# Kernel optimization log

Hardware: AMD Instinct MI355X
Metric: run time of the kernel (lower is better)

The kernel has to match this reference:

```python
import jax, jax.numpy as jnp
import numpy as np

B, P, DE, DD, DA = 256, 196, 2048, 512, 512

def setup_inputs() -> dict:
    key = jax.random.key(0)
    ks = jax.random.split(key, 8)
    s_enc = 1.0 / np.sqrt(DE)
    s_dec = 1.0 / np.sqrt(DD)
    s_att = 1.0 / np.sqrt(DA)
    return {
        "encoder_out": jax.random.normal(ks[0], (B, P, DE), dtype=jnp.float32),
        "decoder_hidden": jax.random.normal(ks[1], (B, DD), dtype=jnp.float32),
        "W_enc": jax.random.uniform(ks[2], (DE, DA), jnp.float32, -s_enc, s_enc),
        "b_enc": jax.random.uniform(ks[3], (DA,), jnp.float32, -s_enc, s_enc),
        "W_dec": jax.random.uniform(ks[4], (DD, DA), jnp.float32, -s_dec, s_dec),
        "b_dec": jax.random.uniform(ks[5], (DA,), jnp.float32, -s_dec, s_dec),
        "W_full": jax.random.uniform(ks[6], (DA, 1), jnp.float32, -s_att, s_att),
        "b_full": jax.random.uniform(ks[7], (1,), jnp.float32, -s_att, s_att),
    }

def reference(encoder_out, decoder_hidden, W_enc, b_enc, W_dec, b_dec, W_full, b_full):
    # att1: [B,P,DA]; att2: [B,DA]
    att1 = jnp.einsum('bpe,ea->bpa', encoder_out, W_enc) + b_enc
    att2 = decoder_hidden @ W_dec + b_dec
    # broadcast add + relu + project to scalar score per position
    att = jnp.einsum('bpa,a->bp', jax.nn.relu(att1 + att2[:, None, :]), W_full[:, 0]) + b_full[0]
    alpha = jax.nn.softmax(att, axis=1)  # [B,P]
    context_vector = jnp.einsum('bpe,bp->be', encoder_out, alpha)  # [B,DE]
    return (context_vector, alpha)
```

## Files before the change

### kernel.cpp

```cpp
#include <hip/hip_runtime.h>
#include <hip/hip_bf16.h>
#include <cstddef>

#define B_   256
#define P_   196
#define DE_  2048
#define DD_  512
#define DA_  512
#define M_   (B_*P_)

#define BM   64
#define KT   32
#define NKT  (DE_/KT)

typedef __attribute__((ext_vector_type(4))) float f32x4;
typedef __attribute__((ext_vector_type(8))) short s16x8;

static __device__ __forceinline__ short f2bf(float x) {
    __hip_bfloat16 h = __float2bfloat16(x);
    return *reinterpret_cast<short*>(&h);
}

__global__ __launch_bounds__(256) void pack_wenc(
        const float* __restrict__ W, __hip_bfloat16* __restrict__ out) {
    __shared__ float lds[KT][DA_];
    const int kt = blockIdx.x;
    const int t  = threadIdx.x;
#pragma unroll
    for (int i = 0; i < 64; ++i) {
        int e = i * 256 + t;
        int k = e >> 9, n = e & 511;
        lds[k][n] = W[(size_t)(kt * KT + k) * DA_ + n];
    }
    __syncthreads();
    short* o = reinterpret_cast<short*>(out) + (size_t)kt * (32 * 64 * 8);
#pragma unroll
    for (int i = 0; i < 8; ++i) {
        int idx  = i * 256 + t;
        int gf   = idx >> 6;
        int lane = idx & 63;
        int g = lane >> 4, c = lane & 15;
        s16x8 w;
#pragma unroll
        for (int j = 0; j < 8; ++j)
            w[j] = f2bf(lds[g * 8 + j][gf * 16 + c]);
        *reinterpret_cast<s16x8*>(o + (size_t)idx * 8) = w;
    }
}

__global__ __launch_bounds__(512) void att2_kernel(
        const float* __restrict__ dh, const float* __restrict__ W_dec,
        const float* __restrict__ b_dec, const float* __restrict__ b_enc,
        float* __restrict__ att2p) {
    __shared__ float s_dh[DD_];
    const int b = blockIdx.x;
    const int a = threadIdx.x;
    s_dh[a] = dh[(size_t)b * DD_ + a];
    __syncthreads();
    float acc = 0.f;
#pragma unroll 8
    for (int k = 0; k < DD_; ++k)
        acc += s_dh[k] * W_dec[(size_t)k * DA_ + a];
    att2p[(size_t)b * DA_ + a] = acc + b_dec[a] + b_enc[a];
}

__global__ __launch_bounds__(256, 2) void gemm_att(
        const float* __restrict__ enc, const __hip_bfloat16* __restrict__ Bp,
        const float* __restrict__ att2p, const float* __restrict__ Wfull,
        const float* __restrict__ bfull, float* __restrict__ att) {
    __shared__ __hip_bfloat16 a_lds0[BM * KT];
    __shared__ __hip_bfloat16 a_lds1[BM * KT];
    __shared__ float red[BM][4];

    const int tid  = threadIdx.x;
    const int wave = tid >> 6;
    const int lane = tid & 63;
    const int g    = lane >> 4;
    const int c    = lane & 15;
    const int block_row = blockIdx.x * BM;
    const int nbase = wave * 128;
    const int slot8 = (g ^ ((c >> 1) & 3)) * 8;

    const int ar = tid >> 2;
    const int aq = tid & 3;
    const int a_woff = ar * KT + (aq ^ ((ar >> 1) & 3)) * 8;
    const float* ap = enc + (size_t)(block_row + ar) * DE_ + aq * 8;

    const s16x8* bp = reinterpret_cast<const s16x8*>(Bp) + (size_t)(wave * 8) * 64 + lane;

    f32x4 acc[4][8] = {};
    f32x4 pX0, pX1, pY0, pY1;
    s16x8 bf[8];

#define ISSUE_A(v0, v1, T) do {                                         \
        const int tt_ = (T) > 63 ? 63 : (T);                            \
        v0 = *reinterpret_cast<const f32x4*>(ap + tt_ * KT);            \
        v1 = *reinterpret_cast<const f32x4*>(ap + tt_ * KT + 4);        \
    } while (0)

#define ISSUE_BF(T) do {                                                \
        _Pragma("unroll")                                               \
        for (int nt_ = 0; nt_ < 8; ++nt_)                               \
            bf[nt_] = bp[((size_t)(T) * 32 + nt_) * 64];                \
    } while (0)

#define STORE_A(dst, v0, v1) do {                                       \
        s16x8 w_;                                                       \
        w_[0]=f2bf((v0).x); w_[1]=f2bf((v0).y); w_[2]=f2bf((v0).z); w_[3]=f2bf((v0).w); \
        w_[4]=f2bf((v1).x); w_[5]=f2bf((v1).y); w_[6]=f2bf((v1).z); w_[7]=f2bf((v1).w); \
        *reinterpret_cast<s16x8*>((dst) + a_woff) = w_;                 \
    } while (0)

#define AFRAGS_MFMA(abuf) do {                                          \
        s16x8 af[4];                                                    \
        _Pragma("unroll")                                               \
        for (int mt_ = 0; mt_ < 4; ++mt_)                               \
            af[mt_] = *reinterpret_cast<const s16x8*>((abuf) + (mt_*16 + c) * KT + slot8); \
        _Pragma("unroll")                                               \
        for (int nt_ = 0; nt_ < 8; ++nt_)                               \
            _Pragma("unroll")                                           \
            for (int mt_ = 0; mt_ < 4; ++mt_)                           \
                acc[mt_][nt_] = __builtin_amdgcn_mfma_f32_16x16x32_bf16(\
                                    af[mt_], bf[nt_], acc[mt_][nt_], 0, 0, 0); \
    } while (0)

#define BAR() do {                                                      \
        asm volatile("s_waitcnt lgkmcnt(0)" ::: "memory");              \
        __builtin_amdgcn_s_barrier();                                   \
        __builtin_amdgcn_sched_barrier(0);                              \
    } while (0)

    ISSUE_A(pX0, pX1, 0);
    ISSUE_A(pY0, pY1, 1);
    ISSUE_BF(0);
    STORE_A(a_lds0, pX0, pX1);
    ISSUE_A(pX0, pX1, 2);
    BAR();

#pragma clang loop unroll(disable)
    for (int t = 0; t < 62; t += 2) {
        STORE_A(a_lds1, pY0, pY1);
        ISSUE_A(pY0, pY1, t + 3);
        AFRAGS_MFMA(a_lds0);
        ISSUE_BF(t + 1);
        BAR();
        STORE_A(a_lds0, pX0, pX1);
        ISSUE_A(pX0, pX1, t + 4);
        AFRAGS_MFMA(a_lds1);
        ISSUE_BF(t + 2);
        BAR();
    }
    STORE_A(a_lds1, pY0, pY1);
    AFRAGS_MFMA(a_lds0);
    ISSUE_BF(63);
    BAR();
    AFRAGS_MFMA(a_lds1);

    const int b0    = block_row / P_;
    const int b1    = min(b0 + 1, B_ - 1);
    const int split = (b0 + 1) * P_;
    float wf[8], a20[8], a21[8];
#pragma unroll
    for (int nt = 0; nt < 8; ++nt) {
        const int n = nbase + nt * 16 + c;
        wf[nt]  = Wfull[n];
        a20[nt] = att2p[(size_t)b0 * DA_ + n];
        a21[nt] = att2p[(size_t)b1 * DA_ + n];
    }
#pragma unroll
    for (int mt = 0; mt < 4; ++mt) {
#pragma unroll
        for (int q = 0; q < 4; ++q) {
            const int row_local = mt * 16 + g * 4 + q;
            const int R = block_row + row_local;
            const bool hi = (R >= split);
            float s = 0.f;
#pragma unroll
            for (int nt = 0; nt < 8; ++nt) {
                float a2 = hi ? a21[nt] : a20[nt];
                float v  = acc[mt][nt][q] + a2;
                v = fmaxf(v, 0.f);
                s += v * wf[nt];
            }
#pragma unroll
            for (int off = 1; off < 16; off <<= 1)
                s += __shfl_xor(s, off, 64);
            if (c == 0) red[row_local][wave] = s;
        }
    }
    __syncthreads();
    if (tid < BM) {
        float t = 0.f;
#pragma unroll
        for (int w = 0; w < 4; ++w) t += red[tid][w];
        att[block_row + tid] = t + bfull[0];
    }
#undef ISSUE_A
#undef ISSUE_BF
#undef STORE_A
#undef AFRAGS_MFMA
#undef BAR
}

__global__ __launch_bounds__(256) void softmax_kernel(
        const float* __restrict__ att, float* __restrict__ alpha) {
    const int b = blockIdx.x;
    const int t = threadIdx.x;
    __shared__ float sred[4];
    float v = (t < P_) ? att[(size_t)b * P_ + t] : -1e30f;
    float m = v;
#pragma unroll
    for (int off = 1; off < 64; off <<= 1) m = fmaxf(m, __shfl_xor(m, off, 64));
    if ((t & 63) == 0) sred[t >> 6] = m;
    __syncthreads();
    const float mall = fmaxf(fmaxf(sred[0], sred[1]), fmaxf(sred[2], sred[3]));
    __syncthreads();
    float e = (t < P_) ? expf(v - mall) : 0.f;
    float s = e;
#pragma unroll
    for (int off = 1; off < 64; off <<= 1) s += __shfl_xor(s, off, 64);
    if ((t & 63) == 0) sred[t >> 6] = s;
    __syncthreads();
    const float stot = sred[0] + sred[1] + sred[2] + sred[3];
    if (t < P_) alpha[(size_t)b * P_ + t] = e / stot;
}

__global__ __launch_bounds__(256) void context_kernel(
        const float* __restrict__ enc, const float* __restrict__ alpha,
        float* __restrict__ ctx) {
    const int b = blockIdx.x;
    const int e = blockIdx.y * 1024 + threadIdx.x * 4;
    __shared__ float s_alpha[P_];
    if (threadIdx.x < P_) s_alpha[threadIdx.x] = alpha[(size_t)b * P_ + threadIdx.x];
    __syncthreads();
    f32x4 acc = {0.f, 0.f, 0.f, 0.f};
    const float* base = enc + (size_t)b * P_ * DE_ + e;
#pragma unroll 4
    for (int p = 0; p < P_; ++p) {
        f32x4 v = *reinterpret_cast<const f32x4*>(base + (size_t)p * DE_);
        acc += s_alpha[p] * v;
    }
    *reinterpret_cast<f32x4*>(ctx + (size_t)b * DE_ + e) = acc;
}

extern "C" void kernel_launch(void* const* d_in, const int* in_sizes, int n_in,
                              void* d_out, int out_size, void* d_ws, size_t ws_size,
                              hipStream_t stream) {
    const float* enc    = (const float*)d_in[0];
    const float* dh     = (const float*)d_in[1];
    const float* W_enc  = (const float*)d_in[2];
    const float* b_enc  = (const float*)d_in[3];
    const float* W_dec  = (const float*)d_in[4];
    const float* b_dec  = (const float*)d_in[5];
    const float* W_full = (const float*)d_in[6];
    const float* b_full = (const float*)d_in[7];

    float* out       = (float*)d_out;
    float* ctx_out   = out;
    float* alpha_out = out + (size_t)B_ * DE_;

    char* ws = (char*)d_ws;
    __hip_bfloat16* Bp = (__hip_bfloat16*)ws;
    float* att2p = (float*)(ws + 2u * 1024 * 1024);
    float* att   = (float*)(ws + 2u * 1024 * 1024 + 512u * 1024);

    pack_wenc   <<<NKT,             256, 0, stream>>>(W_enc, Bp);
    att2_kernel <<<B_,              512, 0, stream>>>(dh, W_dec, b_dec, b_enc, att2p);
    gemm_att    <<<M_ / BM,         256, 0, stream>>>(enc, Bp, att2p, W_full, b_full, att);
    softmax_kernel<<<B_,            256, 0, stream>>>(att, alpha_out);
    context_kernel<<<dim3(B_, 2),   256, 0, stream>>>(enc, alpha_out, ctx_out);
}
```

Baseline: 275.3 us.

## Load A fragments directly from global into registers, dropping LDS staging and barriers

The fused attention GEMM no longer stages the fp32 encoder tile in LDS. Each wave now loads its A fragments straight from global memory into registers, converts them to bf16 and feeds the MFMAs, prefetching A two k-steps ahead and B one step ahead. This removes the LDS writes and reads and the per-step workgroup barriers. In exchange, all four waves of a block fetch and convert the same A rows, quadrupling A requests to L1/L2 on the largest tensor and raising register pressure.

```diff
diff --git a/kernel.cpp b/kernel.cpp
--- a/kernel.cpp
+++ b/kernel.cpp
@@ -68,8 +68,6 @@
         const float* __restrict__ enc, const __hip_bfloat16* __restrict__ Bp,
         const float* __restrict__ att2p, const float* __restrict__ Wfull,
         const float* __restrict__ bfull, float* __restrict__ att) {
-    __shared__ __hip_bfloat16 a_lds0[BM * KT];
-    __shared__ __hip_bfloat16 a_lds1[BM * KT];
     __shared__ float red[BM][4];
 
     const int tid  = threadIdx.x;
@@ -79,82 +77,64 @@
     const int c    = lane & 15;
     const int block_row = blockIdx.x * BM;
     const int nbase = wave * 128;
-    const int slot8 = (g ^ ((c >> 1) & 3)) * 8;
-
-    const int ar = tid >> 2;
-    const int aq = tid & 3;
-    const int a_woff = ar * KT + (aq ^ ((ar >> 1) & 3)) * 8;
-    const float* ap = enc + (size_t)(block_row + ar) * DE_ + aq * 8;
-
+
+    const float* aptr = enc + (size_t)(block_row + c) * DE_ + g * 8;
     const s16x8* bp = reinterpret_cast<const s16x8*>(Bp) + (size_t)(wave * 8) * 64 + lane;
 
     f32x4 acc[4][8] = {};
-    f32x4 pX0, pX1, pY0, pY1;
-    s16x8 bf[8];
-
-#define ISSUE_A(v0, v1, T) do {                                         \
-        const int tt_ = (T) > 63 ? 63 : (T);                            \
-        v0 = *reinterpret_cast<const f32x4*>(ap + tt_ * KT);            \
-        v1 = *reinterpret_cast<const f32x4*>(ap + tt_ * KT + 4);        \
-    } while (0)
-
-#define ISSUE_BF(T) do {                                                \
-        _Pragma("unroll")                                               \
-        for (int nt_ = 0; nt_ < 8; ++nt_)                               \
-            bf[nt_] = bp[((size_t)(T) * 32 + nt_) * 64];                \
-    } while (0)
-
-#define STORE_A(dst, v0, v1) do {                                       \
-        s16x8 w_;                                                       \
-        w_[0]=f2bf((v0).x); w_[1]=f2bf((v0).y); w_[2]=f2bf((v0).z); w_[3]=f2bf((v0).w); \
-        w_[4]=f2bf((v1).x); w_[5]=f2bf((v1).y); w_[6]=f2bf((v1).z); w_[7]=f2bf((v1).w); \
-        *reinterpret_cast<s16x8*>((dst) + a_woff) = w_;                 \
-    } while (0)
-
-#define AFRAGS_MFMA(abuf) do {                                          \
-        s16x8 af[4];                                                    \
-        _Pragma("unroll")                                               \
-        for (int mt_ = 0; mt_ < 4; ++mt_)                               \
-            af[mt_] = *reinterpret_cast<const s16x8*>((abuf) + (mt_*16 + c) * KT + slot8); \
-        _Pragma("unroll")                                               \
-        for (int nt_ = 0; nt_ < 8; ++nt_)                               \
-            _Pragma("unroll")                                           \
-            for (int mt_ = 0; mt_ < 4; ++mt_)                           \
-                acc[mt_][nt_] = __builtin_amdgcn_mfma_f32_16x16x32_bf16(\
+    f32x4 pa[4][2];
+    s16x8 af[4], bf[8];
+
+#define LOAD_A_T(T) do {                                                 \
+        _Pragma("unroll")                                                \
+        for (int mt_ = 0; mt_ < 4; ++mt_) {                              \
+            const float* p_ = aptr + (size_t)mt_ * (16 * DE_) + (T) * KT;\
+            pa[mt_][0] = *reinterpret_cast<const f32x4*>(p_);            \
+            pa[mt_][1] = *reinterpret_cast<const f32x4*>(p_ + 4);        \
+        }                                                                \
+    } while (0)
+
+#define CVT_A() do {                                                     \
+        _Pragma("unroll")                                                \
+        for (int mt_ = 0; mt_ < 4; ++mt_) {                              \
+            s16x8 w_;                                                    \
+            w_[0]=f2bf(pa[mt_][0].x); w_[1]=f2bf(pa[mt_][0].y);          \
+            w_[2]=f2bf(pa[mt_][0].z); w_[3]=f2bf(pa[mt_][0].w);          \
+            w_[4]=f2bf(pa[mt_][1].x); w_[5]=f2bf(pa[mt_][1].y);          \
+            w_[6]=f2bf(pa[mt_][1].z); w_[7]=f2bf(pa[mt_][1].w);          \
+            af[mt_] = w_;                                                \
+        }                                                                \
+    } while (0)
+
+#define LOAD_B_T(T) do {                                                 \
+        _Pragma("unroll")                                                \
+        for (int nt_ = 0; nt_ < 8; ++nt_)                                \
+            bf[nt_] = bp[(size_t)(T) * 2048 + nt_ * 64];                 \
+    } while (0)
+
+#define MFMA_STEP() do {                                                 \
+        _Pragma("unroll")                                                \
+        for (int nt_ = 0; nt_ < 8; ++nt_)                                \
+            _Pragma("unroll")                                            \
+            for (int mt_ = 0; mt_ < 4; ++mt_)                            \
+                acc[mt_][nt_] = __builtin_amdgcn_mfma_f32_16x16x32_bf16( \
                                     af[mt_], bf[nt_], acc[mt_][nt_], 0, 0, 0); \
     } while (0)
 
-#define BAR() do {                                                      \
-        asm volatile("s_waitcnt lgkmcnt(0)" ::: "memory");              \
-        __builtin_amdgcn_s_barrier();                                   \
-        __builtin_amdgcn_sched_barrier(0);                              \
-    } while (0)
-
-    ISSUE_A(pX0, pX1, 0);
-    ISSUE_A(pY0, pY1, 1);
-    ISSUE_BF(0);
-    STORE_A(a_lds0, pX0, pX1);
-    ISSUE_A(pX0, pX1, 2);
-    BAR();
+    LOAD_A_T(0);
+    LOAD_B_T(0);
+    CVT_A();
+    LOAD_A_T(1);
 
 #pragma clang loop unroll(disable)
-    for (int t = 0; t < 62; t += 2) {
-        STORE_A(a_lds1, pY0, pY1);
-        ISSUE_A(pY0, pY1, t + 3);
-        AFRAGS_MFMA(a_lds0);
-        ISSUE_BF(t + 1);
-        BAR();
-        STORE_A(a_lds0, pX0, pX1);
-        ISSUE_A(pX0, pX1, t + 4);
-        AFRAGS_MFMA(a_lds1);
-        ISSUE_BF(t + 2);
-        BAR();
-    }
-    STORE_A(a_lds1, pY0, pY1);
-    AFRAGS_MFMA(a_lds0);
-    ISSUE_BF(63);
-    BAR();
-    AFRAGS_MFMA(a_lds1);
+    for (int t = 0; t < NKT; ++t) {
+        MFMA_STEP();
+        const int t1 = (t + 1 < NKT) ? t + 1 : NKT - 1;
+        const int t2 = (t + 2 < NKT) ? t + 2 : NKT - 1;
+        LOAD_B_T(t1);
+        CVT_A();
+        LOAD_A_T(t2);
+    }
 
     const int b0    = block_row / P_;
     const int b1    = min(b0 + 1, B_ - 1);
@@ -195,11 +175,10 @@
         for (int w = 0; w < 4; ++w) t += red[tid][w];
         att[block_row + tid] = t + bfull[0];
     }
-#undef ISSUE_A
-#undef ISSUE_BF
-#undef STORE_A
-#undef AFRAGS_MFMA
-#undef BAR
+#undef LOAD_A_T
+#undef CVT_A
+#undef LOAD_B_T
+#undef MFMA_STEP
 }
 
 __global__ __launch_bounds__(256) void softmax_kernel(
```

Measured after the change: 445.6 us. 1.62x slower.

## Split GEMM N dimension across two blocks with partial score buffers

Applied to the files above, without the earlier changes.

The fused attention GEMM now splits the 512-wide DA dimension into two halves handled by separate blocks, doubling the grid and halving per-block accumulators (acc 4x4). Each half writes partial scores to its own buffer, and the softmax sums them; b_full is dropped because a constant shift does not change softmax. Blocks are ordered so pairs of blocks sharing the same row tile run close together for L2 reuse of the encoder rows. B fragments are double-buffered one step further ahead, and occupancy is raised to 3 blocks/CU. The cost is that the fp32 encoder rows are read and converted twice, once per N-half.

```diff
diff --git a/kernel.cpp b/kernel.cpp
--- a/kernel.cpp
+++ b/kernel.cpp
@@ -64,10 +64,10 @@
     att2p[(size_t)b * DA_ + a] = acc + b_dec[a] + b_enc[a];
 }
 
-__global__ __launch_bounds__(256, 2) void gemm_att(
+__global__ __launch_bounds__(256, 3) void gemm_att(
         const float* __restrict__ enc, const __hip_bfloat16* __restrict__ Bp,
         const float* __restrict__ att2p, const float* __restrict__ Wfull,
-        const float* __restrict__ bfull, float* __restrict__ att) {
+        float* __restrict__ att0, float* __restrict__ att1) {
     __shared__ __hip_bfloat16 a_lds0[BM * KT];
     __shared__ __hip_bfloat16 a_lds1[BM * KT];
     __shared__ float red[BM][4];
@@ -77,8 +77,12 @@
     const int lane = tid & 63;
     const int g    = lane >> 4;
     const int c    = lane & 15;
-    const int block_row = blockIdx.x * BM;
-    const int nbase = wave * 128;
+
+    const int p   = blockIdx.x;
+    const int mt_ = (p >> 4) * 8 + (p & 7);
+    const int nh  = (p >> 3) & 1;
+    const int block_row = mt_ * BM;
+
     const int slot8 = (g ^ ((c >> 1) & 3)) * 8;
 
     const int ar = tid >> 2;
@@ -86,83 +90,85 @@
     const int a_woff = ar * KT + (aq ^ ((ar >> 1) & 3)) * 8;
     const float* ap = enc + (size_t)(block_row + ar) * DE_ + aq * 8;
 
-    const s16x8* bp = reinterpret_cast<const s16x8*>(Bp) + (size_t)(wave * 8) * 64 + lane;
-
-    f32x4 acc[4][8] = {};
+    const s16x8* bp = reinterpret_cast<const s16x8*>(Bp)
+                    + ((size_t)(nh * 16 + wave * 4)) * 64 + lane;
+
+    f32x4 acc[4][4] = {};
     f32x4 pX0, pX1, pY0, pY1;
-    s16x8 bf[8];
-
-#define ISSUE_A(v0, v1, T) do {                                         \
-        const int tt_ = (T) > 63 ? 63 : (T);                            \
-        v0 = *reinterpret_cast<const f32x4*>(ap + tt_ * KT);            \
-        v1 = *reinterpret_cast<const f32x4*>(ap + tt_ * KT + 4);        \
-    } while (0)
-
-#define ISSUE_BF(T) do {                                                \
-        _Pragma("unroll")                                               \
-        for (int nt_ = 0; nt_ < 8; ++nt_)                               \
-            bf[nt_] = bp[((size_t)(T) * 32 + nt_) * 64];                \
-    } while (0)
-
-#define STORE_A(dst, v0, v1) do {                                       \
-        s16x8 w_;                                                       \
+    s16x8 bfX[4], bfY[4];
+
+#define ISSUE_A(v0, v1, T) do {                                          \
+        const int tt_ = (T) > 63 ? 63 : (T);                             \
+        v0 = *reinterpret_cast<const f32x4*>(ap + tt_ * KT);             \
+        v1 = *reinterpret_cast<const f32x4*>(ap + tt_ * KT + 4);         \
+    } while (0)
+
+#define ISSUE_B(dst, T) do {                                             \
+        _Pragma("unroll")                                                \
+        for (int nt_ = 0; nt_ < 4; ++nt_)                                \
+            dst[nt_] = bp[((size_t)(T) * 32 + nt_) * 64];                \
+    } while (0)
+
+#define STORE_A(dst, v0, v1) do {                                        \
+        s16x8 w_;                                                        \
         w_[0]=f2bf((v0).x); w_[1]=f2bf((v0).y); w_[2]=f2bf((v0).z); w_[3]=f2bf((v0).w); \
         w_[4]=f2bf((v1).x); w_[5]=f2bf((v1).y); w_[6]=f2bf((v1).z); w_[7]=f2bf((v1).w); \
-        *reinterpret_cast<s16x8*>((dst) + a_woff) = w_;                 \
-    } while (0)
-
-#define AFRAGS_MFMA(abuf) do {                                          \
-        s16x8 af[4];                                                    \
-        _Pragma("unroll")                                               \
-        for (int mt_ = 0; mt_ < 4; ++mt_)                               \
-            af[mt_] = *reinterpret_cast<const s16x8*>((abuf) + (mt_*16 + c) * KT + slot8); \
-        _Pragma("unroll")                                               \
-        for (int nt_ = 0; nt_ < 8; ++nt_)                               \
-            _Pragma("unroll")                                           \
-            for (int mt_ = 0; mt_ < 4; ++mt_)                           \
-                acc[mt_][nt_] = __builtin_amdgcn_mfma_f32_16x16x32_bf16(\
-                                    af[mt_], bf[nt_], acc[mt_][nt_], 0, 0, 0); \
-    } while (0)
-
-#define BAR() do {                                                      \
-        asm volatile("s_waitcnt lgkmcnt(0)" ::: "memory");              \
-        __builtin_amdgcn_s_barrier();                                   \
-        __builtin_amdgcn_sched_barrier(0);                              \
+        *reinterpret_cast<s16x8*>((dst) + a_woff) = w_;                  \
+    } while (0)
+
+#define FRAGS_MFMA(abuf, bfr) do {                                       \
+        s16x8 af[4];                                                     \
+        _Pragma("unroll")                                                \
+        for (int mt2 = 0; mt2 < 4; ++mt2)                                \
+            af[mt2] = *reinterpret_cast<const s16x8*>((abuf) + (mt2*16 + c) * KT + slot8); \
+        _Pragma("unroll")                                                \
+        for (int nt2 = 0; nt2 < 4; ++nt2)                                \
+            _Pragma("unroll")                                            \
+            for (int mt2 = 0; mt2 < 4; ++mt2)                            \
+                acc[mt2][nt2] = __builtin_amdgcn_mfma_f32_16x16x32_bf16( \
+                                    af[mt2], bfr[nt2], acc[mt2][nt2], 0, 0, 0); \
+    } while (0)
+
+#define BAR() do {                                                       \
+        asm volatile("s_waitcnt lgkmcnt(0)" ::: "memory");               \
+        __builtin_amdgcn_s_barrier();                                    \
+        __builtin_amdgcn_sched_barrier(0);                               \
     } while (0)
 
     ISSUE_A(pX0, pX1, 0);
     ISSUE_A(pY0, pY1, 1);
-    ISSUE_BF(0);
+    ISSUE_B(bfX, 0);
     STORE_A(a_lds0, pX0, pX1);
     ISSUE_A(pX0, pX1, 2);
+    ISSUE_B(bfY, 1);
     BAR();
 
 #pragma clang loop unroll(disable)
     for (int t = 0; t < 62; t += 2) {
         STORE_A(a_lds1, pY0, pY1);
         ISSUE_A(pY0, pY1, t + 3);
-        AFRAGS_MFMA(a_lds0);
-        ISSUE_BF(t + 1);
+        FRAGS_MFMA(a_lds0, bfX);
+        ISSUE_B(bfX, t + 2);
         BAR();
         STORE_A(a_lds0, pX0, pX1);
         ISSUE_A(pX0, pX1, t + 4);
-        AFRAGS_MFMA(a_lds1);
-        ISSUE_BF(t + 2);
+        FRAGS_MFMA(a_lds1, bfY);
+        ISSUE_B(bfY, t + 3);
         BAR();
     }
     STORE_A(a_lds1, pY0, pY1);
-    AFRAGS_MFMA(a_lds0);
-    ISSUE_BF(63);
+    FRAGS_MFMA(a_lds0, bfX);
     BAR();
-    AFRAGS_MFMA(a_lds1);
+    FRAGS_MFMA(a_lds1, bfY);
 
     const int b0    = block_row / P_;
     const int b1    = min(b0 + 1, B_ - 1);
     const int split = (b0 + 1) * P_;
-    float wf[8], a20[8], a21[8];
-#pragma unroll
-    for (int nt = 0; nt < 8; ++nt) {
-        const int n = nbase + nt * 16 + c;
+    const int ncol0 = nh * 256 + wave * 64;
+    float wf[4], a20[4], a21[4];
+#pragma unroll
+    for (int nt = 0; nt < 4; ++nt) {
+        const int n = ncol0 + nt * 16 + c;
         wf[nt]  = Wfull[n];
         a20[nt] = att2p[(size_t)b0 * DA_ + n];
         a21[nt] = att2p[(size_t)b1 * DA_ + n];
@@ -176,7 +182,7 @@
             const bool hi = (R >= split);
             float s = 0.f;
 #pragma unroll
-            for (int nt = 0; nt < 8; ++nt) {
+            for (int nt = 0; nt < 4; ++nt) {
                 float a2 = hi ? a21[nt] : a20[nt];
                 float v  = acc[mt][nt][q] + a2;
                 v = fmaxf(v, 0.f);
@@ -190,24 +196,25 @@
     }
     __syncthreads();
     if (tid < BM) {
-        float t = 0.f;
-#pragma unroll
-        for (int w = 0; w < 4; ++w) t += red[tid][w];
-        att[block_row + tid] = t + bfull[0];
+        float t = red[tid][0] + red[tid][1] + red[tid][2] + red[tid][3];
+        float* dst = nh ? att1 : att0;
+        dst[block_row + tid] = t;
     }
 #undef ISSUE_A
-#undef ISSUE_BF
+#undef ISSUE_B
 #undef STORE_A
-#undef AFRAGS_MFMA
+#undef FRAGS_MFMA
 #undef BAR
 }
 
 __global__ __launch_bounds__(256) void softmax_kernel(
-        const float* __restrict__ att, float* __restrict__ alpha) {
+        const float* __restrict__ att0, const float* __restrict__ att1,
+        float* __restrict__ alpha) {
     const int b = blockIdx.x;
     const int t = threadIdx.x;
     __shared__ float sred[4];
-    float v = (t < P_) ? att[(size_t)b * P_ + t] : -1e30f;
+    float v = -1e30f;
+    if (t < P_) v = att0[(size_t)b * P_ + t] + att1[(size_t)b * P_ + t];
     float m = v;
 #pragma unroll
     for (int off = 1; off < 64; off <<= 1) m = fmaxf(m, __shfl_xor(m, off, 64));
@@ -253,7 +260,6 @@
     const float* W_dec  = (const float*)d_in[4];
     const float* b_dec  = (const float*)d_in[5];
     const float* W_full = (const float*)d_in[6];
-    const float* b_full = (const float*)d_in[7];
 
     float* out       = (float*)d_out;
     float* ctx_out   = out;
@@ -262,11 +268,12 @@
     char* ws = (char*)d_ws;
     __hip_bfloat16* Bp = (__hip_bfloat16*)ws;
     float* att2p = (float*)(ws + 2u * 1024 * 1024);
-    float* att   = (float*)(ws + 2u * 1024 * 1024 + 512u * 1024);
-
-    pack_wenc   <<<NKT,             256, 0, stream>>>(W_enc, Bp);
-    att2_kernel <<<B_,              512, 0, stream>>>(dh, W_dec, b_dec, b_enc, att2p);
-    gemm_att    <<<M_ / BM,         256, 0, stream>>>(enc, Bp, att2p, W_full, b_full, att);
-    softmax_kernel<<<B_,            256, 0, stream>>>(att, alpha_out);
-    context_kernel<<<dim3(B_, 2),   256, 0, stream>>>(enc, alpha_out, ctx_out);
-}
+    float* att0  = (float*)(ws + 2u * 1024 * 1024 + 512u * 1024);
+    float* att1  = att0 + M_;
+
+    pack_wenc     <<<NKT,            256, 0, stream>>>(W_enc, Bp);
+    att2_kernel   <<<B_,             512, 0, stream>>>(dh, W_dec, b_dec, b_enc, att2p);
+    gemm_att      <<<2 * (M_ / BM),  256, 0, stream>>>(enc, Bp, att2p, W_full, att0, att1);
+    softmax_kernel<<<B_,             256, 0, stream>>>(att0, att1, alpha_out);
+    context_kernel<<<dim3(B_, 2),    256, 0, stream>>>(enc, alpha_out, ctx_out);
+}
```

Result: no change. 279.8 us (+1.6%).
